# Kernel tuning notes

Hardware: AMD Instinct MI355X
Metric: run time of the kernel (lower is better)

Reference implementation:

```python
import jax, jax.numpy as jnp
import numpy as np

N = 8192
STEPS = 10        # num_propagation_steps
ALPHA = 0.5       # self-retention parameter
LR = 0.01         # learning_rate for the M update
EPS = 1e-10


def setup_inputs() -> dict:
    key = jax.random.key(0)
    k1, k2 = jax.random.split(key)
    adj_matrix = jax.random.uniform(k1, (N, N), dtype=jnp.float32)  # dense non-negative adjacency
    positive_nodes = jax.random.bernoulli(k2, 0.5, (N,)).astype(jnp.float32)  # binary labels
    M = jnp.ones((N, N), dtype=jnp.float32)  # nn.Parameter initialized to ones
    return {"adj_matrix": adj_matrix, "positive_nodes": positive_nodes, "M": M}


def _propagation_loss(adj, pos):
    # degree_matrix @ adj @ degree_matrix with diagonal degree matrix ==
    # row/column scaling by deg^{-1/2} (same math, no O(N^3) diag GEMMs)
    d = jnp.power(adj.sum(axis=1), -0.5)          # [N]
    diffusion = d[:, None] * adj * d[None, :]     # [N, N]
    cp = jnp.stack([1.0 - pos, pos], axis=1)      # [N, 2] class posterior

    def step(cp, _):
        cp = ALPHA * (diffusion @ cp) + (1.0 - ALPHA) * cp
        return cp, None

    cp, _ = jax.lax.scan(step, cp, None, length=STEPS)
    # mean of -log(1 - neg_prob + eps) over nodes where positive_nodes == 1
    neg = cp[:, 0]
    loss = -(pos * jnp.log(1.0 - neg + EPS)).sum() / pos.sum()
    return loss


def reference(adj_matrix, positive_nodes, M):
    loss = _propagation_loss(adj_matrix, positive_nodes)
    # In the original, loss.backward() populates M.grad; since the loss does not
    # depend on M, dLoss/dM == 0, so M_new = M - LR * 0 = M (math-equivalent).
    updated_adj = M * adj_matrix
    return updated_adj, loss
```

## Files before the change

kernel.cpp:

```cpp
#include <hip/hip_runtime.h>
#include <hip/hip_bf16.h>

#define NN 8192
constexpr int   STEPS = 10;
constexpr float ALPHA = 0.5f;
constexpr float EPSV  = 1e-10f;

typedef float f32x2 __attribute__((ext_vector_type(2)));
typedef float f32x4 __attribute__((ext_vector_type(4)));

static __device__ __forceinline__ unsigned int f2bf(float f) {
    unsigned int u = __float_as_uint(f);
    return (u + 0x7FFFu + ((u >> 16) & 1u)) >> 16;
}
static __device__ __forceinline__ float bf2f(unsigned int h) {
    return __uint_as_float(h << 16);
}

__global__ __launch_bounds__(256) void k_fused_prep(
        const float* __restrict__ adj, const float* __restrict__ M,
        float* __restrict__ out, unsigned char* __restrict__ a8,
        float* __restrict__ rowsum) {
    const int row = blockIdx.x;
    const int t   = threadIdx.x;
    const float* arow = adj + (size_t)row * NN;
    const float* mrow = M   + (size_t)row * NN;
    float*       orow = out + (size_t)row * NN;
    unsigned char* brow = a8 + (size_t)row * NN;
    float acc = 0.0f;
#pragma unroll
    for (int g = 0; g < 2; ++g) {
        f32x4 v[4], m[4];
#pragma unroll
        for (int k = 0; k < 4; ++k) {
            const int j = (g * 4 + k) * 1024 + t * 4;
            v[k] = __builtin_nontemporal_load((const f32x4*)(arow + j));
        }
#pragma unroll
        for (int k = 0; k < 4; ++k) {
            const int j = (g * 4 + k) * 1024 + t * 4;
            m[k] = __builtin_nontemporal_load((const f32x4*)(mrow + j));
        }
#pragma unroll
        for (int k = 0; k < 4; ++k) {
            const int j = (g * 4 + k) * 1024 + t * 4;
            f32x4 r = v[k] * m[k];
            __builtin_nontemporal_store(r, (f32x4*)(orow + j));
            acc += (v[k].x + v[k].y) + (v[k].z + v[k].w);
            int p = __builtin_amdgcn_cvt_pk_fp8_f32(v[k].x, v[k].y, 0, false);
            p     = __builtin_amdgcn_cvt_pk_fp8_f32(v[k].z, v[k].w, p, true);
            *(unsigned int*)(brow + j) = (unsigned int)p;
        }
    }
#pragma unroll
    for (int o = 32; o > 0; o >>= 1) acc += __shfl_down(acc, o);
    __shared__ float red[4];
    if ((t & 63) == 0) red[t >> 6] = acc;
    __syncthreads();
    if (t == 0) rowsum[row] = (red[0] + red[1]) + (red[2] + red[3]);
}

#define CBLK  256
#define CROWS 32

static __device__ __forceinline__ void gbar(unsigned int* flags, unsigned int phase) {
    __syncthreads();
    if (threadIdx.x == 0)
        __hip_atomic_store(&flags[blockIdx.x], phase, __ATOMIC_RELEASE,
                           __HIP_MEMORY_SCOPE_AGENT);
    while (__hip_atomic_load(&flags[threadIdx.x], __ATOMIC_ACQUIRE,
                             __HIP_MEMORY_SCOPE_AGENT) < phase)
        __builtin_amdgcn_s_sleep(1);
    __syncthreads();
}

#define FMA_WORD(w, base)                                             \
    { f32x2 lo = __builtin_amdgcn_cvt_pk_f32_fp8((int)(w), false);    \
      f32x2 hi = __builtin_amdgcn_cvt_pk_f32_fp8((int)(w), true);     \
      a0 = fmaf(lo[0], zf[(base) + 0], a0);                           \
      a1 = fmaf(lo[1], zf[(base) + 1], a1);                           \
      a0 = fmaf(hi[0], zf[(base) + 2], a0);                           \
      a1 = fmaf(hi[1], zf[(base) + 3], a1); }

__global__ __launch_bounds__(256, 1) void k_chain(
        const unsigned char* __restrict__ a8, const float* __restrict__ rowsum,
        const float* __restrict__ pos,
        unsigned int* __restrict__ z_a, unsigned int* __restrict__ z_b,
        unsigned int* __restrict__ flags, float* __restrict__ accs,
        float* __restrict__ loss_out) {
    const int t  = threadIdx.x;
    const int b  = blockIdx.x;
    const int r0 = b * CROWS;
    __shared__ float xloc[CROWS], dloc[CROWS], ploc[CROWS];
    __shared__ unsigned short zs[CROWS];
    __shared__ float red[CROWS][4];

    if (t < CROWS) {
        const int row = r0 + t;
        const float dv = rsqrtf(rowsum[row]);
        const float pv = pos[row];
        const float xv = 1.0f - pv;
        dloc[t] = dv; ploc[t] = pv; xloc[t] = xv;
        zs[t] = (unsigned short)f2bf(dv * xv);
    }
    __syncthreads();
    if (t < CROWS / 2) {
        unsigned int w = (unsigned)zs[2 * t] | ((unsigned)zs[2 * t + 1] << 16);
        __hip_atomic_store(&z_a[r0 / 2 + t], w, __ATOMIC_RELAXED,
                           __HIP_MEMORY_SCOPE_AGENT);
    }
    gbar(flags, 1u);

    const int j = t * 32;
    uint4 pa[CROWS][2];
#pragma unroll
    for (int r = 0; r < CROWS; ++r) {
        const unsigned char* arow = a8 + (size_t)(r0 + r) * NN + j;
        pa[r][0] = *(const uint4*)(arow);
        pa[r][1] = *(const uint4*)(arow + 16);
    }

    const unsigned int* zi = z_a;
    unsigned int*       zo = z_b;
#pragma unroll 1
    for (int s = 0; s < STEPS; ++s) {
        float zf[32];
#pragma unroll
        for (int k = 0; k < 16; ++k) {
            unsigned int q = __hip_atomic_load(&zi[(j >> 1) + k], __ATOMIC_RELAXED,
                                               __HIP_MEMORY_SCOPE_AGENT);
            zf[2 * k]     = bf2f(q & 0xFFFFu);
            zf[2 * k + 1] = bf2f(q >> 16);
        }
        float acc[CROWS];
#pragma unroll
        for (int r = 0; r < CROWS; ++r) {
            float a0 = 0.0f, a1 = 0.0f;
            FMA_WORD(pa[r][0].x,  0) FMA_WORD(pa[r][0].y,  4)
            FMA_WORD(pa[r][0].z,  8) FMA_WORD(pa[r][0].w, 12)
            FMA_WORD(pa[r][1].x, 16) FMA_WORD(pa[r][1].y, 20)
            FMA_WORD(pa[r][1].z, 24) FMA_WORD(pa[r][1].w, 28)
            acc[r] = a0 + a1;
        }
#pragma unroll
        for (int r = 0; r < CROWS; ++r) {
#pragma unroll
            for (int o = 32; o > 0; o >>= 1) acc[r] += __shfl_down(acc[r], o);
        }
        if ((t & 63) == 0) {
            const int w = t >> 6;
#pragma unroll
            for (int r = 0; r < CROWS; ++r) red[r][w] = acc[r];
        }
        __syncthreads();
        if (t < CROWS) {
            const float y  = (red[t][0] + red[t][1]) + (red[t][2] + red[t][3]);
            const float dv = dloc[t];
            const float xn = ALPHA * dv * y + (1.0f - ALPHA) * xloc[t];
            xloc[t] = xn;
            zs[t] = (unsigned short)f2bf(dv * xn);
        }
        __syncthreads();
        if (s < STEPS - 1) {
            if (t < CROWS / 2) {
                unsigned int w = (unsigned)zs[2 * t] | ((unsigned)zs[2 * t + 1] << 16);
                __hip_atomic_store(&zo[r0 / 2 + t], w, __ATOMIC_RELAXED,
                                   __HIP_MEMORY_SCOPE_AGENT);
            }
            gbar(flags, (unsigned)(2 + s));
            const unsigned int* tz = zi; zi = zo; zo = (unsigned int*)tz;
        }
    }

    if (t < CROWS) {
        const float xn = xloc[t];
        red[t][0] = ploc[t] * logf(1.0f - xn + EPSV);
        red[t][1] = ploc[t];
    }
    __syncthreads();
    if (t == 0) {
        float n = 0.0f, dd = 0.0f;
#pragma unroll
        for (int r = 0; r < CROWS; ++r) { n += red[r][0]; dd += red[r][1]; }
        atomicAdd(&accs[0], n);
        atomicAdd(&accs[1], dd);
        unsigned int tk = __hip_atomic_fetch_add((unsigned int*)&accs[2], 1u,
                                                 __ATOMIC_ACQ_REL,
                                                 __HIP_MEMORY_SCOPE_AGENT);
        if (tk == CBLK - 1) {
            float sn = __hip_atomic_load(&accs[0], __ATOMIC_RELAXED,
                                         __HIP_MEMORY_SCOPE_AGENT);
            float sd = __hip_atomic_load(&accs[1], __ATOMIC_RELAXED,
                                         __HIP_MEMORY_SCOPE_AGENT);
            loss_out[0] = -sn / sd;
        }
    }
}

__global__ __launch_bounds__(256) void k_rowsum(
        const float* __restrict__ adj, float* __restrict__ rowsum) {
    const int row = blockIdx.x;
    const int t   = threadIdx.x;
    const float* arow = adj + (size_t)row * NN;
    float acc = 0.0f;
#pragma unroll
    for (int c = 0; c < 8; ++c) {
        const int j = c * 1024 + t * 4;
        float4 v = *(const float4*)(arow + j);
        acc += (v.x + v.y) + (v.z + v.w);
    }
#pragma unroll
    for (int o = 32; o > 0; o >>= 1) acc += __shfl_down(acc, o);
    __shared__ float red[4];
    if ((t & 63) == 0) red[t >> 6] = acc;
    __syncthreads();
    if (t == 0) rowsum[row] = (red[0] + red[1]) + (red[2] + red[3]);
}

__global__ __launch_bounds__(256) void k_init(
        const float* __restrict__ rowsum, const float* __restrict__ pos,
        float* __restrict__ d, float* __restrict__ x,
        unsigned short* __restrict__ zbf, float* __restrict__ zf) {
    const int i = blockIdx.x * 256 + threadIdx.x;
    const float dv = rsqrtf(rowsum[i]);
    const float xv = 1.0f - pos[i];
    const float zv = dv * xv;
    d[i] = dv;
    x[i] = xv;
    zbf[i] = (unsigned short)f2bf(zv);
    zf[i] = zv;
}

__global__ __launch_bounds__(256) void k_step_fp8(
        const unsigned char* __restrict__ a8, const float* __restrict__ d,
        const float* __restrict__ xin, const unsigned short* __restrict__ zin,
        float* __restrict__ xout, unsigned short* __restrict__ zout) {
    const int r0 = blockIdx.x * 4;
    const int t  = threadIdx.x;
    const int j  = t * 32;

    uint4 pa[4][2];
#pragma unroll
    for (int r = 0; r < 4; ++r) {
        const unsigned char* arow = a8 + (size_t)(r0 + r) * NN + j;
        pa[r][0] = *(const uint4*)(arow);
        pa[r][1] = *(const uint4*)(arow + 16);
    }
    uint4 zp[4];
#pragma unroll
    for (int k = 0; k < 4; ++k)
        zp[k] = *(const uint4*)(zin + j + 8 * k);

    float acc0 = 0.0f, acc1 = 0.0f, acc2 = 0.0f, acc3 = 0.0f;
#pragma unroll
    for (int h = 0; h < 2; ++h) {
        float zf[16];
#pragma unroll
        for (int k = 0; k < 2; ++k) {
            uint4 q = zp[2 * h + k];
            zf[k * 8 + 0] = bf2f(q.x & 0xFFFFu); zf[k * 8 + 1] = bf2f(q.x >> 16);
            zf[k * 8 + 2] = bf2f(q.y & 0xFFFFu); zf[k * 8 + 3] = bf2f(q.y >> 16);
            zf[k * 8 + 4] = bf2f(q.z & 0xFFFFu); zf[k * 8 + 5] = bf2f(q.z >> 16);
            zf[k * 8 + 6] = bf2f(q.w & 0xFFFFu); zf[k * 8 + 7] = bf2f(q.w >> 16);
        }
#pragma unroll
        for (int r = 0; r < 4; ++r) {
            const uint4 p = pa[r][h];
            unsigned int w[4] = {p.x, p.y, p.z, p.w};
            float a = 0.0f;
#pragma unroll
            for (int wi = 0; wi < 4; ++wi) {
                f32x2 lo = __builtin_amdgcn_cvt_pk_f32_fp8((int)w[wi], false);
                f32x2 hi = __builtin_amdgcn_cvt_pk_f32_fp8((int)w[wi], true);
                a = fmaf(lo[0], zf[wi * 4 + 0], a);
                a = fmaf(lo[1], zf[wi * 4 + 1], a);
                a = fmaf(hi[0], zf[wi * 4 + 2], a);
                a = fmaf(hi[1], zf[wi * 4 + 3], a);
            }
            if (r == 0) acc0 += a; else if (r == 1) acc1 += a;
            else if (r == 2) acc2 += a; else acc3 += a;
        }
    }
#pragma unroll
    for (int o = 32; o > 0; o >>= 1) {
        acc0 += __shfl_down(acc0, o);
        acc1 += __shfl_down(acc1, o);
        acc2 += __shfl_down(acc2, o);
        acc3 += __shfl_down(acc3, o);
    }
    __shared__ float red[4][4];
    if ((t & 63) == 0) {
        const int w = t >> 6;
        red[0][w] = acc0; red[1][w] = acc1; red[2][w] = acc2; red[3][w] = acc3;
    }
    __syncthreads();
    if (t < 4) {
        const int row = r0 + t;
        const float y  = (red[t][0] + red[t][1]) + (red[t][2] + red[t][3]);
        const float dv = d[row];
        const float xn = ALPHA * dv * y + (1.0f - ALPHA) * xin[row];
        xout[row] = xn;
        zout[row] = (unsigned short)f2bf(dv * xn);
    }
}

__global__ __launch_bounds__(256) void k_step_f32(
        const float* __restrict__ adj, const float* __restrict__ d,
        const float* __restrict__ xin, const float* __restrict__ zin,
        float* __restrict__ xout, float* __restrict__ zout) {
    const int row = blockIdx.x;
    const int t   = threadIdx.x;
    const float* arow = adj + (size_t)row * NN;
    float acc = 0.0f;
#pragma unroll
    for (int c = 0; c < 8; ++c) {
        const int j = c * 1024 + t * 4;
        float4 a = *(const float4*)(arow + j);
        float4 z = *(const float4*)(zin + j);
        acc = fmaf(a.x, z.x, acc); acc = fmaf(a.y, z.y, acc);
        acc = fmaf(a.z, z.z, acc); acc = fmaf(a.w, z.w, acc);
    }
#pragma unroll
    for (int o = 32; o > 0; o >>= 1) acc += __shfl_down(acc, o);
    __shared__ float red[4];
    if ((t & 63) == 0) red[t >> 6] = acc;
    __syncthreads();
    if (t == 0) {
        const float y  = (red[0] + red[1]) + (red[2] + red[3]);
        const float dv = d[row];
        const float xn = ALPHA * dv * y + (1.0f - ALPHA) * xin[row];
        xout[row] = xn;
        zout[row] = dv * xn;
    }
}

__global__ __launch_bounds__(256) void k_mul(
        const float* __restrict__ adj, const float* __restrict__ M,
        float* __restrict__ out) {
    size_t i = ((size_t)blockIdx.x * blockDim.x + threadIdx.x) * 4;
    const size_t stride = (size_t)gridDim.x * blockDim.x * 4;
    const size_t total = (size_t)NN * NN;
    for (; i < total; i += stride) {
        float4 a = *(const float4*)(adj + i);
        float4 m = *(const float4*)(M + i);
        float4 r;
        r.x = a.x * m.x; r.y = a.y * m.y; r.z = a.z * m.z; r.w = a.w * m.w;
        *(float4*)(out + i) = r;
    }
}

__global__ __launch_bounds__(1024) void k_loss(
        const float* __restrict__ pos, const float* __restrict__ xfin,
        float* __restrict__ out) {
    const int t = threadIdx.x;
    float sn = 0.0f, sd = 0.0f;
#pragma unroll
    for (int c = 0; c < 8; ++c) {
        const int i4 = c * 1024 + t;
        float4 p = *(const float4*)(pos  + i4 * 4);
        float4 x = *(const float4*)(xfin + i4 * 4);
        sn += p.x * logf(1.0f - x.x + EPSV);
        sn += p.y * logf(1.0f - x.y + EPSV);
        sn += p.z * logf(1.0f - x.z + EPSV);
        sn += p.w * logf(1.0f - x.w + EPSV);
        sd += (p.x + p.y) + (p.z + p.w);
    }
#pragma unroll
    for (int o = 32; o > 0; o >>= 1) {
        sn += __shfl_down(sn, o);
        sd += __shfl_down(sd, o);
    }
    __shared__ float rn[16], rd[16];
    if ((t & 63) == 0) { rn[t >> 6] = sn; rd[t >> 6] = sd; }
    __syncthreads();
    if (t == 0) {
        float n = 0.0f, dd = 0.0f;
#pragma unroll
        for (int k = 0; k < 16; ++k) { n += rn[k]; dd += rd[k]; }
        out[0] = -n / dd;
    }
}

extern "C" void kernel_launch(void* const* d_in, const int* in_sizes, int n_in,
                              void* d_out, int out_size, void* d_ws, size_t ws_size,
                              hipStream_t stream) {
    const float* adj = (const float*)d_in[0];
    const float* pos = (const float*)d_in[1];
    const float* M   = (const float*)d_in[2];
    float* out = (float*)d_out;

    char* ws = (char*)d_ws;
    float* d_vec  = (float*)(ws + 0);
    float* rowsum = (float*)(ws + 32768);
    float* x_a    = (float*)(ws + 65536);
    float* x_b    = (float*)(ws + 98304);
    unsigned short* zb_a = (unsigned short*)(ws + 131072);
    unsigned short* zb_b = (unsigned short*)(ws + 163840);
    unsigned int* flags  = (unsigned int*)(ws + 196608);
    float*        accs   = (float*)(ws + 196608 + 4096);
    float* zf_a   = (float*)(ws + 196608);
    float* zf_b   = (float*)(ws + 229376);
    unsigned char* a8 = (unsigned char*)(ws + 262144);

    const size_t need_fp8 = 262144 + (size_t)NN * NN;
    const bool use_fp8 = (ws_size >= need_fp8);

    static int s_chain = -1;
    if (s_chain < 0) {
        int nb = 0, ncu = 0;
        hipError_t e1 = hipOccupancyMaxActiveBlocksPerMultiprocessor(&nb, k_chain, 256, 0);
        hipError_t e2 = hipDeviceGetAttribute(&ncu, hipDeviceAttributeMultiprocessorCount, 0);
        s_chain = (e1 == hipSuccess && e2 == hipSuccess && nb >= 1 && nb * ncu >= CBLK) ? 1 : 0;
    }

    if (use_fp8) {
        k_fused_prep<<<NN, 256, 0, stream>>>(adj, M, out, a8, rowsum);
    } else {
        k_rowsum<<<NN, 256, 0, stream>>>(adj, rowsum);
    }

    if (use_fp8 && s_chain == 1) {
        hipMemsetAsync(flags, 0, 4096 + 64, stream);
        k_chain<<<CBLK, 256, 0, stream>>>(a8, rowsum, pos,
                                          (unsigned int*)zb_a, (unsigned int*)zb_b,
                                          flags, accs, out + (size_t)NN * NN);
        return;
    }

    k_init<<<NN / 256, 256, 0, stream>>>(rowsum, pos, d_vec, x_a, zb_a, zf_a);
    float* xi = x_a; float* xo = x_b;
    unsigned short* zbi = zb_a; unsigned short* zbo = zb_b;
    float* zfi = zf_a; float* zfo = zf_b;
    for (int s = 0; s < STEPS; ++s) {
        if (use_fp8) {
            k_step_fp8<<<NN / 4, 256, 0, stream>>>(a8, d_vec, xi, zbi, xo, zbo);
            unsigned short* tz = zbi; zbi = zbo; zbo = tz;
        } else {
            k_step_f32<<<NN, 256, 0, stream>>>(adj, d_vec, xi, zfi, xo, zfo);
            float* tz = zfi; zfi = zfo; zfo = tz;
        }
        float* t = xi; xi = xo; xo = t;
    }
    if (!use_fp8) {
        k_mul<<<2048, 256, 0, stream>>>(adj, M, out);
    }
    k_loss<<<1, 1024, 0, stream>>>(pos, xi, out + (size_t)NN * NN);
}
```

Before: 261.5 us.

## Split resident adjacency tile between registers and swizzled LDS, vectorize z loads

Half of each block's 32 fp8 adjacency rows stay in registers and the other half move into a 128KB LDS buffer with an XOR swizzle. The rows are re-read from LDS on every propagation step. The z vector is now read with plain vector loads instead of per-word atomic loads, and the FMAs use packed f32x2 math. The goal is to cut register pressure and spills, at the cost of extra LDS traffic per step and a very large LDS allocation.

```diff
diff --git a/kernel.cpp b/kernel.cpp
--- a/kernel.cpp
+++ b/kernel.cpp
@@ -62,6 +62,8 @@
 
 #define CBLK  256
 #define CROWS 32
+#define RREG  16
+#define RLDS  16
 
 static __device__ __forceinline__ void gbar(unsigned int* flags, unsigned int phase) {
     __syncthreads();
@@ -74,13 +76,21 @@
     __syncthreads();
 }
 
-#define FMA_WORD(w, base)                                             \
+static __device__ __forceinline__ int lds_off(int r, int c) {
+    return r * 8192 + ((c ^ ((c >> 3) & 7)) << 4);
+}
+
+#define FMA_WORD(w, m)                                                \
     { f32x2 lo = __builtin_amdgcn_cvt_pk_f32_fp8((int)(w), false);    \
       f32x2 hi = __builtin_amdgcn_cvt_pk_f32_fp8((int)(w), true);     \
-      a0 = fmaf(lo[0], zf[(base) + 0], a0);                           \
-      a1 = fmaf(lo[1], zf[(base) + 1], a1);                           \
-      a0 = fmaf(hi[0], zf[(base) + 2], a0);                           \
-      a1 = fmaf(hi[1], zf[(base) + 3], a1); }
+      a01 += lo * zf2[(m)];                                           \
+      a23 += hi * zf2[(m) + 1]; }
+
+#define DOT_ROW(q0, q1, res)                                                        \
+    { f32x2 a01 = {0.f, 0.f}, a23 = {0.f, 0.f};                                     \
+      FMA_WORD(q0.x, 0)  FMA_WORD(q0.y, 2)  FMA_WORD(q0.z, 4)  FMA_WORD(q0.w, 6)   \
+      FMA_WORD(q1.x, 8)  FMA_WORD(q1.y, 10) FMA_WORD(q1.z, 12) FMA_WORD(q1.w, 14)  \
+      res = (a01[0] + a01[1]) + (a23[0] + a23[1]); }
 
 __global__ __launch_bounds__(256, 1) void k_chain(
         const unsigned char* __restrict__ a8, const float* __restrict__ rowsum,
@@ -91,6 +101,8 @@
     const int t  = threadIdx.x;
     const int b  = blockIdx.x;
     const int r0 = b * CROWS;
+
+    __shared__ __align__(16) unsigned char lds_a[RLDS * 8192];
     __shared__ float xloc[CROWS], dloc[CROWS], ploc[CROWS];
     __shared__ unsigned short zs[CROWS];
     __shared__ float red[CROWS][4];
@@ -109,48 +121,88 @@
         __hip_atomic_store(&z_a[r0 / 2 + t], w, __ATOMIC_RELAXED,
                            __HIP_MEMORY_SCOPE_AGENT);
     }
-    gbar(flags, 1u);
 
     const int j = t * 32;
-    uint4 pa[CROWS][2];
-#pragma unroll
-    for (int r = 0; r < CROWS; ++r) {
+    uint4 pa[RREG][2];
+#pragma unroll
+    for (int r = 0; r < RREG; ++r) {
         const unsigned char* arow = a8 + (size_t)(r0 + r) * NN + j;
         pa[r][0] = *(const uint4*)(arow);
         pa[r][1] = *(const uint4*)(arow + 16);
     }
+#pragma unroll
+    for (int g = 0; g < 4; ++g) {
+        uint4 v0[4], v1[4];
+#pragma unroll
+        for (int rr = 0; rr < 4; ++rr) {
+            const unsigned char* arow =
+                a8 + (size_t)(r0 + RREG + g * 4 + rr) * NN + j;
+            v0[rr] = *(const uint4*)(arow);
+            v1[rr] = *(const uint4*)(arow + 16);
+        }
+#pragma unroll
+        for (int rr = 0; rr < 4; ++rr) {
+            const int lr = g * 4 + rr;
+            *(uint4*)&lds_a[lds_off(lr, 2 * t)]     = v0[rr];
+            *(uint4*)&lds_a[lds_off(lr, 2 * t + 1)] = v1[rr];
+        }
+    }
+    gbar(flags, 1u);
 
     const unsigned int* zi = z_a;
     unsigned int*       zo = z_b;
 #pragma unroll 1
     for (int s = 0; s < STEPS; ++s) {
-        float zf[32];
-#pragma unroll
-        for (int k = 0; k < 16; ++k) {
-            unsigned int q = __hip_atomic_load(&zi[(j >> 1) + k], __ATOMIC_RELAXED,
-                                               __HIP_MEMORY_SCOPE_AGENT);
-            zf[2 * k]     = bf2f(q & 0xFFFFu);
-            zf[2 * k + 1] = bf2f(q >> 16);
-        }
-        float acc[CROWS];
-#pragma unroll
-        for (int r = 0; r < CROWS; ++r) {
-            float a0 = 0.0f, a1 = 0.0f;
-            FMA_WORD(pa[r][0].x,  0) FMA_WORD(pa[r][0].y,  4)
-            FMA_WORD(pa[r][0].z,  8) FMA_WORD(pa[r][0].w, 12)
-            FMA_WORD(pa[r][1].x, 16) FMA_WORD(pa[r][1].y, 20)
-            FMA_WORD(pa[r][1].z, 24) FMA_WORD(pa[r][1].w, 28)
-            acc[r] = a0 + a1;
-        }
-#pragma unroll
-        for (int r = 0; r < CROWS; ++r) {
-#pragma unroll
-            for (int o = 32; o > 0; o >>= 1) acc[r] += __shfl_down(acc[r], o);
+        f32x2 zf2[16];
+        {
+            const uint4* zv = (const uint4*)(zi + t * 16);
+            uint4 zq[4];
+#pragma unroll
+            for (int k = 0; k < 4; ++k) zq[k] = zv[k];
+#pragma unroll
+            for (int k = 0; k < 4; ++k) {
+                const unsigned int ww[4] = {zq[k].x, zq[k].y, zq[k].z, zq[k].w};
+#pragma unroll
+                for (int m = 0; m < 4; ++m) {
+                    f32x2 p;
+                    p[0] = bf2f(ww[m] & 0xFFFFu);
+                    p[1] = bf2f(ww[m] >> 16);
+                    zf2[k * 4 + m] = p;
+                }
+            }
+        }
+        float accA[RREG];
+#pragma unroll
+        for (int r = 0; r < RREG; ++r) {
+            DOT_ROW(pa[r][0], pa[r][1], accA[r]);
+        }
+#pragma unroll
+        for (int r = 0; r < RREG; ++r) {
+#pragma unroll
+            for (int o = 32; o > 0; o >>= 1) accA[r] += __shfl_down(accA[r], o);
         }
         if ((t & 63) == 0) {
             const int w = t >> 6;
 #pragma unroll
-            for (int r = 0; r < CROWS; ++r) red[r][w] = acc[r];
+            for (int r = 0; r < RREG; ++r) red[r][w] = accA[r];
+        }
+        float accB[RLDS];
+#pragma unroll
+        for (int r = 0; r < RLDS; ++r) {
+            const uint4 q0 = *(const uint4*)&lds_a[lds_off(r, 2 * t)];
+            const uint4 q1 = *(const uint4*)&lds_a[lds_off(r, 2 * t + 1)];
+            DOT_ROW(q0, q1, accB[r]);
+            if ((r & 3) == 3) __builtin_amdgcn_sched_barrier(0);
+        }
+#pragma unroll
+        for (int r = 0; r < RLDS; ++r) {
+#pragma unroll
+            for (int o = 32; o > 0; o >>= 1) accB[r] += __shfl_down(accB[r], o);
+        }
+        if ((t & 63) == 0) {
+            const int w = t >> 6;
+#pragma unroll
+            for (int r = 0; r < RLDS; ++r) red[RREG + r][w] = accB[r];
         }
         __syncthreads();
         if (t < CROWS) {
```

Result: no change. 261.0 us (-0.2%).
